# Kernel optimization log

Measured on AMD Instinct MI355X. Metric: run time of the kernel, lower is better.

## Reference

```python
import jax, jax.numpy as jnp
import numpy as np

ACT_BITS = 7      # activation - 1 (symmetric signed quantization)
WEIGHT_BITS = 7   # weight - 1
LN_EPS = 1e-5


def t_quantize(x, k):
    # Symmetric per-tensor uniform quantization to k bits with STE.
    # q = round(clip(x/s, -1, 1) * (2^k - 1)) / (2^k - 1) * s, s = max|x|
    n = float(2 ** k - 1)
    s = jnp.maximum(jnp.max(jnp.abs(x)), 1e-12)
    q = jnp.round(jnp.clip(x / s, -1.0, 1.0) * n) / n * s
    return x + jax.lax.stop_gradient(q - x)  # straight-through


def layer_norm(x, gamma, beta):
    mu = jnp.mean(x, axis=-1, keepdims=True)
    var = jnp.mean(jnp.square(x - mu), axis=-1, keepdims=True)
    return (x - mu) * jax.lax.rsqrt(var + LN_EPS) * gamma + beta


def ir_linear(x, w, b):
    # IRlinear: linear with per-tensor quantized weights (STE).
    wq = t_quantize(w, WEIGHT_BITS)
    return jnp.einsum('bsd,hd->bsh', x, wq) + b


def setup_inputs() -> dict:
    key = jax.random.key(0)
    ks = jax.random.split(key, 4)
    dim, hidden = 1024, 4096
    B, S = 4, 8192
    return {
        'x': jax.random.normal(ks[0], (B, S, dim), dtype=jnp.float32),
        'gamma': jnp.ones((dim,), jnp.float32),
        'beta': jnp.zeros((dim,), jnp.float32),
        'w1': jax.random.normal(ks[1], (hidden, dim), jnp.float32) * (1.0 / np.sqrt(dim)),
        'b1': jnp.zeros((hidden,), jnp.float32),
        'w2': jax.random.normal(ks[2], (dim, hidden), jnp.float32) * (1.0 / np.sqrt(hidden)),
        'b2': jnp.zeros((dim,), jnp.float32),
    }


def reference(x, gamma, beta, w1, b1, w2, b2):
    # x = T_quantize(LayerNorm(x), activation-1)
    h = t_quantize(layer_norm(x, gamma, beta), ACT_BITS)
    # x = T_quantize(GELU(IRlinear1(x)), activation-1)  (exact erf GELU, torch default)
    h = t_quantize(jax.nn.gelu(ir_linear(h, w1, b1), approximate=False), ACT_BITS)
    # net[3:] = Dropout(0) -> IRlinear2 -> Dropout(0)
    return ir_linear(h, w2, b2)
```

## Files before the change

kernel.cpp:

```cpp
#include <hip/hip_runtime.h>
#include <stdint.h>

typedef int v4i __attribute__((ext_vector_type(4)));

#define GLD_LDS16(g, l) __builtin_amdgcn_global_load_lds( \
    (const __attribute__((address_space(1))) void*)(g),   \
    (__attribute__((address_space(3))) void*)(l), 16, 0, 0)

__device__ __forceinline__ float wsum(float v){
  #pragma unroll
  for (int o = 32; o; o >>= 1) v += __shfl_xor(v, o, 64);
  return v;
}
__device__ __forceinline__ float wmaxr(float v){
  #pragma unroll
  for (int o = 32; o; o >>= 1) v = fmaxf(v, __shfl_xor(v, o, 64));
  return v;
}
__device__ __forceinline__ float gelu_f(float x){
  return 0.5f * x * (1.0f + erff(x * 0.7071067811865476f));
}

__global__ __launch_bounds__(256) void k_ln_absmax(
    const float* __restrict__ x, const float* __restrict__ gamma,
    const float* __restrict__ beta, unsigned int* __restrict__ smax_out, int M)
{
  __shared__ float red[4];
  const int lane = threadIdx.x & 63, wave = threadIdx.x >> 6;
  float lmax = 0.f;
  for (int row = blockIdx.x * 4 + wave; row < M; row += gridDim.x * 4) {
    const float4* xr = (const float4*)(x + (size_t)row * 1024);
    float4 v[4]; float s = 0.f;
    #pragma unroll
    for (int j = 0; j < 4; j++){ v[j] = xr[j*64 + lane]; s += v[j].x+v[j].y+v[j].z+v[j].w; }
    s = wsum(s);
    const float mu = s * (1.f/1024.f);
    float sq = 0.f;
    #pragma unroll
    for (int j = 0; j < 4; j++){
      float a=v[j].x-mu, b=v[j].y-mu, c=v[j].z-mu, d=v[j].w-mu;
      sq += a*a + b*b + c*c + d*d;
    }
    sq = wsum(sq);
    const float rs = 1.0f / sqrtf(sq * (1.f/1024.f) + 1e-5f);
    #pragma unroll
    for (int j = 0; j < 4; j++){
      int c0 = j*256 + lane*4;
      float4 g = *(const float4*)(gamma + c0);
      float4 b = *(const float4*)(beta + c0);
      float y0=(v[j].x-mu)*rs*g.x+b.x, y1=(v[j].y-mu)*rs*g.y+b.y;
      float y2=(v[j].z-mu)*rs*g.z+b.z, y3=(v[j].w-mu)*rs*g.w+b.w;
      lmax = fmaxf(lmax, fmaxf(fmaxf(fabsf(y0),fabsf(y1)), fmaxf(fabsf(y2),fabsf(y3))));
    }
  }
  lmax = wmaxr(lmax);
  if (lane == 0) red[wave] = lmax;
  __syncthreads();
  if (threadIdx.x == 0)
    atomicMax(smax_out, __float_as_uint(fmaxf(fmaxf(red[0],red[1]), fmaxf(red[2],red[3]))));
}

__global__ __launch_bounds__(256) void k_ln_quant(
    const float* __restrict__ x, const float* __restrict__ gamma,
    const float* __restrict__ beta, const unsigned int* __restrict__ sbits,
    signed char* __restrict__ A1, int M)
{
  const float s = fmaxf(__uint_as_float(*sbits), 1e-12f);
  const int lane = threadIdx.x & 63, wave = threadIdx.x >> 6;
  for (int row = blockIdx.x * 4 + wave; row < M; row += gridDim.x * 4) {
    const float4* xr = (const float4*)(x + (size_t)row * 1024);
    float4 v[4]; float sm = 0.f;
    #pragma unroll
    for (int j = 0; j < 4; j++){ v[j] = xr[j*64 + lane]; sm += v[j].x+v[j].y+v[j].z+v[j].w; }
    sm = wsum(sm);
    const float mu = sm * (1.f/1024.f);
    float sq = 0.f;
    #pragma unroll
    for (int j = 0; j < 4; j++){
      float a=v[j].x-mu, b=v[j].y-mu, c=v[j].z-mu, d=v[j].w-mu;
      sq += a*a + b*b + c*c + d*d;
    }
    sq = wsum(sq);
    const float rs = 1.0f / sqrtf(sq * (1.f/1024.f) + 1e-5f);
    #pragma unroll
    for (int j = 0; j < 4; j++){
      int c0 = j*256 + lane*4;
      float4 g = *(const float4*)(gamma + c0);
      float4 b = *(const float4*)(beta + c0);
      float y0=(v[j].x-mu)*rs*g.x+b.x, y1=(v[j].y-mu)*rs*g.y+b.y;
      float y2=(v[j].z-mu)*rs*g.z+b.z, y3=(v[j].w-mu)*rs*g.w+b.w;
      char4 qc;
      qc.x = (signed char)(int)rintf(fminf(fmaxf(y0/s,-1.f),1.f)*127.f);
      qc.y = (signed char)(int)rintf(fminf(fmaxf(y1/s,-1.f),1.f)*127.f);
      qc.z = (signed char)(int)rintf(fminf(fmaxf(y2/s,-1.f),1.f)*127.f);
      qc.w = (signed char)(int)rintf(fminf(fmaxf(y3/s,-1.f),1.f)*127.f);
      *(char4*)(A1 + (size_t)row*1024 + c0) = qc;
    }
  }
}

__global__ __launch_bounds__(256) void k_absmax(
    const float* __restrict__ w, long n4, unsigned int* __restrict__ out)
{
  __shared__ float red[4];
  const int lane = threadIdx.x & 63, wave = threadIdx.x >> 6;
  float lmax = 0.f;
  for (long i = blockIdx.x*256 + threadIdx.x; i < n4; i += (long)gridDim.x*256) {
    float4 v = ((const float4*)w)[i];
    lmax = fmaxf(lmax, fmaxf(fmaxf(fabsf(v.x),fabsf(v.y)), fmaxf(fabsf(v.z),fabsf(v.w))));
  }
  lmax = wmaxr(lmax);
  if (lane == 0) red[wave] = lmax;
  __syncthreads();
  if (threadIdx.x == 0)
    atomicMax(out, __float_as_uint(fmaxf(fmaxf(red[0],red[1]), fmaxf(red[2],red[3]))));
}

__global__ __launch_bounds__(256) void k_wquant(
    const float* __restrict__ w, long n4, const unsigned int* __restrict__ sbits,
    signed char* __restrict__ wq)
{
  const float s = fmaxf(__uint_as_float(*sbits), 1e-12f);
  for (long i = blockIdx.x*256 + threadIdx.x; i < n4; i += (long)gridDim.x*256) {
    float4 v = ((const float4*)w)[i];
    char4 qc;
    qc.x = (signed char)(int)rintf(fminf(fmaxf(v.x/s,-1.f),1.f)*127.f);
    qc.y = (signed char)(int)rintf(fminf(fmaxf(v.y/s,-1.f),1.f)*127.f);
    qc.z = (signed char)(int)rintf(fminf(fmaxf(v.z/s,-1.f),1.f)*127.f);
    qc.w = (signed char)(int)rintf(fminf(fmaxf(v.w/s,-1.f),1.f)*127.f);
    *(char4*)(wq + i*4) = qc;
  }
}

template<int MODE>
__global__ __launch_bounds__(256, 2) void k_gemm_i8(
    const signed char* __restrict__ A, const signed char* __restrict__ W,
    const float* __restrict__ bias, const unsigned int* __restrict__ scales,
    float* __restrict__ outf, signed char* __restrict__ outq,
    unsigned int* __restrict__ gmax,
    int M, int N, int K, int ia, int iw, int ig)
{
  __shared__ __align__(16) signed char As[128*64];
  __shared__ __align__(16) signed char Bs[128*64];
  __shared__ float red[4];

  const int nwg = gridDim.x, orig = blockIdx.x;
  const int q8 = nwg >> 3, r8 = nwg & 7;
  const int xcd = orig & 7, idx = orig >> 3;
  const int wgid = (xcd < r8 ? xcd*(q8+1) : r8*(q8+1) + (xcd-r8)*q8) + idx;

  const int tn = N >> 7;
  const int bm = wgid / tn, bn = wgid % tn;
  const int tid = threadIdx.x, lane = tid & 63, wave = tid >> 6;
  const int wm = wave >> 1, wn = wave & 1;
  const size_t row0 = (size_t)bm * 128, col0 = (size_t)bn * 128;

  v4i acc[4][4];
  #pragma unroll
  for (int i = 0; i < 4; i++)
    #pragma unroll
    for (int j = 0; j < 4; j++) acc[i][j] = (v4i){0,0,0,0};

  const int ksteps = K >> 6;
  for (int kt = 0; kt < ksteps; ++kt) {
    const size_t kb = (size_t)kt << 6;
    #pragma unroll
    for (int i = 0; i < 2; i++) {
      const int chunk = i*4 + wave;
      const int off = chunk*1024 + lane*16;
      const int r = off >> 6, kk = off & 63;
      GLD_LDS16(A + (row0 + r)*(size_t)K + kb + kk, As + chunk*1024);
      GLD_LDS16(W + (col0 + r)*(size_t)K + kb + kk, Bs + chunk*1024);
    }
    __syncthreads();

    v4i af[4], bf[4];
    #pragma unroll
    for (int mi = 0; mi < 4; mi++)
      af[mi] = *(const v4i*)(As + ((wm*64 + mi*16 + (lane & 15)) << 6) + ((lane >> 4) << 4));
    #pragma unroll
    for (int ni = 0; ni < 4; ni++)
      bf[ni] = *(const v4i*)(Bs + ((wn*64 + ni*16 + (lane & 15)) << 6) + ((lane >> 4) << 4));
    #pragma unroll
    for (int mi = 0; mi < 4; mi++)
      #pragma unroll
      for (int ni = 0; ni < 4; ni++)
        acc[mi][ni] = __builtin_amdgcn_mfma_i32_16x16x64_i8(af[mi], bf[ni], acc[mi][ni], 0, 0, 0);
    __syncthreads();
  }

  const float sa = fmaxf(__uint_as_float(scales[ia]), 1e-12f);
  const float sw = fmaxf(__uint_as_float(scales[iw]), 1e-12f);
  const float sc = (sa / 127.f) * (sw / 127.f);
  const int rowbase = (int)row0 + wm*64;
  const int colbase = (int)col0 + wn*64;

  if (MODE == 0) {
    float lmax = 0.f;
    #pragma unroll
    for (int mi = 0; mi < 4; mi++)
      #pragma unroll
      for (int ni = 0; ni < 4; ni++) {
        const int colc = colbase + ni*16 + (lane & 15);
        const float b = bias[colc];
        #pragma unroll
        for (int j = 0; j < 4; j++) {
          float g = gelu_f((float)acc[mi][ni][j] * sc + b);
          lmax = fmaxf(lmax, fabsf(g));
        }
      }
    lmax = wmaxr(lmax);
    if (lane == 0) red[wave] = lmax;
    __syncthreads();
    if (tid == 0)
      atomicMax(gmax, __float_as_uint(fmaxf(fmaxf(red[0],red[1]), fmaxf(red[2],red[3]))));
  } else if (MODE == 1) {
    const float sg = fmaxf(__uint_as_float(scales[ig]), 1e-12f);
    #pragma unroll
    for (int mi = 0; mi < 4; mi++)
      #pragma unroll
      for (int ni = 0; ni < 4; ni++) {
        const int colc = colbase + ni*16 + (lane & 15);
        const float b = bias[colc];
        #pragma unroll
        for (int j = 0; j < 4; j++) {
          const int row = rowbase + mi*16 + ((lane >> 4) << 2) + j;
          float g = gelu_f((float)acc[mi][ni][j] * sc + b);
          float t = fminf(fmaxf(g / sg, -1.f), 1.f) * 127.f;
          outq[(size_t)row * N + colc] = (signed char)(int)rintf(t);
        }
      }
  } else {
    #pragma unroll
    for (int mi = 0; mi < 4; mi++)
      #pragma unroll
      for (int ni = 0; ni < 4; ni++) {
        const int colc = colbase + ni*16 + (lane & 15);
        const float b = bias[colc];
        #pragma unroll
        for (int j = 0; j < 4; j++) {
          const int row = rowbase + mi*16 + ((lane >> 4) << 2) + j;
          outf[(size_t)row * N + colc] = (float)acc[mi][ni][j] * sc + b;
        }
      }
  }
}

extern "C" void kernel_launch(void* const* d_in, const int* in_sizes, int n_in,
                              void* d_out, int out_size, void* d_ws, size_t ws_size,
                              hipStream_t stream)
{
  const float* x     = (const float*)d_in[0];
  const float* gamma = (const float*)d_in[1];
  const float* beta  = (const float*)d_in[2];
  const float* w1    = (const float*)d_in[3];
  const float* b1    = (const float*)d_in[4];
  const float* w2    = (const float*)d_in[5];
  const float* b2    = (const float*)d_in[6];
  float* out = (float*)d_out;

  const int D = 1024;
  const int M = in_sizes[0] / D;
  const int H = in_sizes[3] / D;

  char* ws = (char*)d_ws;
  unsigned int* scales = (unsigned int*)ws;
  signed char* A1  = (signed char*)(ws + 256);
  signed char* w1q = A1 + (size_t)M * D;
  signed char* w2q = w1q + (size_t)H * D;
  signed char* A2  = w2q + (size_t)H * D;

  hipMemsetAsync(scales, 0, 32, stream);
  k_absmax<<<512, 256, 0, stream>>>(w1, (long)H * D / 4, scales + 1);
  k_absmax<<<512, 256, 0, stream>>>(w2, (long)H * D / 4, scales + 2);
  k_ln_absmax<<<4096, 256, 0, stream>>>(x, gamma, beta, scales, M);
  k_wquant<<<512, 256, 0, stream>>>(w1, (long)H * D / 4, scales + 1, w1q);
  k_wquant<<<512, 256, 0, stream>>>(w2, (long)H * D / 4, scales + 2, w2q);
  k_ln_quant<<<4096, 256, 0, stream>>>(x, gamma, beta, scales, A1, M);

  const int g1 = (M / 128) * (H / 128);
  k_gemm_i8<0><<<g1, 256, 0, stream>>>(A1, w1q, b1, scales, nullptr, nullptr,
                                       scales + 3, M, H, D, 0, 1, 0);
  k_gemm_i8<1><<<g1, 256, 0, stream>>>(A1, w1q, b1, scales, nullptr, A2,
                                       nullptr, M, H, D, 0, 1, 3);
  const int g2 = (M / 128) * (D / 128);
  k_gemm_i8<2><<<g2, 256, 0, stream>>>(A2, w2q, b2, scales, out, nullptr,
                                       nullptr, M, D, H, 3, 2, 0);
}
```

Before: 1.042 ms.

## Double-buffer int8 GEMM LDS tiles and XOR-swizzle to avoid bank conflicts

The int8 MFMA GEMM main loop now uses two LDS buffers, so global-to-LDS loads for the next K tile are issued while MFMAs run on the current tile. This replaces the two syncthreads per step with one vmcnt wait plus barrier. The LDS layout also gets an XOR swizzle of the 16-byte column chunk by row, meant to reduce bank conflicts on fragment reads. Doubling LDS to about 32KB per block may lower occupancy, and the loop assumes an even number of K steps.

```diff
diff --git a/kernel.cpp b/kernel.cpp
--- a/kernel.cpp
+++ b/kernel.cpp
@@ -140,8 +140,10 @@
     unsigned int* __restrict__ gmax,
     int M, int N, int K, int ia, int iw, int ig)
 {
-  __shared__ __align__(16) signed char As[128*64];
-  __shared__ __align__(16) signed char Bs[128*64];
+  __shared__ __align__(16) signed char As0[128*64];
+  __shared__ __align__(16) signed char Bs0[128*64];
+  __shared__ __align__(16) signed char As1[128*64];
+  __shared__ __align__(16) signed char Bs1[128*64];
   __shared__ float red[4];
 
   const int nwg = gridDim.x, orig = blockIdx.x;
@@ -161,33 +163,68 @@
     #pragma unroll
     for (int j = 0; j < 4; j++) acc[i][j] = (v4i){0,0,0,0};
 
+  int st_r[2], st_kk[2], st_ch[2];
+  #pragma unroll
+  for (int i = 0; i < 2; i++) {
+    const int chunk = i*4 + wave;
+    const int off = chunk*1024 + lane*16;
+    const int r = off >> 6;
+    const int c = (off >> 4) & 3;
+    st_r[i]  = r;
+    st_kk[i] = (c ^ ((r >> 1) & 3)) << 4;
+    st_ch[i] = chunk*1024;
+  }
+  const signed char* Ab = A + row0 * (size_t)K;
+  const signed char* Wb = W + col0 * (size_t)K;
+
+  #define STAGE(AS_, BS_, kb_) do {                                         \
+    _Pragma("unroll")                                                       \
+    for (int i_ = 0; i_ < 2; i_++) {                                        \
+      GLD_LDS16(Ab + (size_t)st_r[i_]*K + (kb_) + st_kk[i_], (AS_) + st_ch[i_]); \
+      GLD_LDS16(Wb + (size_t)st_r[i_]*K + (kb_) + st_kk[i_], (BS_) + st_ch[i_]); \
+    }                                                                       \
+  } while (0)
+
+  #define COMPUTE(AS_, BS_) do {                                            \
+    v4i af_[4], bf_[4];                                                     \
+    const int cf_ = lane >> 4;                                              \
+    _Pragma("unroll")                                                       \
+    for (int mi_ = 0; mi_ < 4; mi_++) {                                     \
+      const int rr_ = wm*64 + mi_*16 + (lane & 15);                         \
+      af_[mi_] = *(const v4i*)((AS_) + (rr_ << 6) + ((cf_ ^ ((rr_ >> 1) & 3)) << 4)); \
+    }                                                                       \
+    _Pragma("unroll")                                                       \
+    for (int ni_ = 0; ni_ < 4; ni_++) {                                     \
+      const int rr_ = wn*64 + ni_*16 + (lane & 15);                         \
+      bf_[ni_] = *(const v4i*)((BS_) + (rr_ << 6) + ((cf_ ^ ((rr_ >> 1) & 3)) << 4)); \
+    }                                                                       \
+    _Pragma("unroll")                                                       \
+    for (int mi_ = 0; mi_ < 4; mi_++)                                       \
+      _Pragma("unroll")                                                     \
+      for (int ni_ = 0; ni_ < 4; ni_++)                                     \
+        acc[mi_][ni_] = __builtin_amdgcn_mfma_i32_16x16x64_i8(af_[mi_], bf_[ni_], acc[mi_][ni_], 0, 0, 0); \
+  } while (0)
+
+  #define VWAIT_BAR() do {                                                  \
+    asm volatile("s_waitcnt vmcnt(0)" ::: "memory");                        \
+    __builtin_amdgcn_s_barrier();                                           \
+  } while (0)
+
   const int ksteps = K >> 6;
-  for (int kt = 0; kt < ksteps; ++kt) {
-    const size_t kb = (size_t)kt << 6;
-    #pragma unroll
-    for (int i = 0; i < 2; i++) {
-      const int chunk = i*4 + wave;
-      const int off = chunk*1024 + lane*16;
-      const int r = off >> 6, kk = off & 63;
-      GLD_LDS16(A + (row0 + r)*(size_t)K + kb + kk, As + chunk*1024);
-      GLD_LDS16(W + (col0 + r)*(size_t)K + kb + kk, Bs + chunk*1024);
-    }
-    __syncthreads();
-
-    v4i af[4], bf[4];
-    #pragma unroll
-    for (int mi = 0; mi < 4; mi++)
-      af[mi] = *(const v4i*)(As + ((wm*64 + mi*16 + (lane & 15)) << 6) + ((lane >> 4) << 4));
-    #pragma unroll
-    for (int ni = 0; ni < 4; ni++)
-      bf[ni] = *(const v4i*)(Bs + ((wn*64 + ni*16 + (lane & 15)) << 6) + ((lane >> 4) << 4));
-    #pragma unroll
-    for (int mi = 0; mi < 4; mi++)
-      #pragma unroll
-      for (int ni = 0; ni < 4; ni++)
-        acc[mi][ni] = __builtin_amdgcn_mfma_i32_16x16x64_i8(af[mi], bf[ni], acc[mi][ni], 0, 0, 0);
-    __syncthreads();
-  }
+  STAGE(As0, Bs0, 0);
+  VWAIT_BAR();
+
+  for (int kt = 0; kt < ksteps; kt += 2) {
+    STAGE(As1, Bs1, ((size_t)(kt + 1)) << 6);
+    COMPUTE(As0, Bs0);
+    VWAIT_BAR();
+    if (kt + 2 < ksteps) STAGE(As0, Bs0, ((size_t)(kt + 2)) << 6);
+    COMPUTE(As1, Bs1);
+    if (kt + 2 < ksteps) VWAIT_BAR();
+  }
+  #undef STAGE
+  #undef COMPUTE
+  #undef VWAIT_BAR
 
   const float sa = fmaxf(__uint_as_float(scales[ia]), 1e-12f);
   const float sw = fmaxf(__uint_as_float(scales[iw]), 1e-12f);
```

After: 1.061 ms. Within noise of the previous version (+1.8%).
